# Optimization experiments

Measured on AMD Instinct MI355X. Metric: run time of the kernel, lower is better.

Reference implementation:

```python
import jax, jax.numpy as jnp
import numpy as np

N = 50000      # nodes
E = 800000     # edges (before self-loops)
IN, HID, HEADS, OUT = 128, 16, 8, 64
NEG_SLOPE = 0.2
EPS = 1e-16


def gat_layer(x, edge_index, W, att_src, att_dst, bias, heads, ch, num_nodes, concat):
    # x: [N, F_in]; edge_index: [2, E'] (row0 = source j, row1 = target i)
    h = (x @ W).reshape(-1, heads, ch)                     # [N, H, C]
    a_src = jnp.sum(h * att_src, axis=-1)                  # [N, H]
    a_dst = jnp.sum(h * att_dst, axis=-1)                  # [N, H]
    src, dst = edge_index[0], edge_index[1]
    alpha = a_src[src] + a_dst[dst]                        # [E', H]
    alpha = jax.nn.leaky_relu(alpha, NEG_SLOPE)
    # segment softmax over incoming edges of each target node
    m = jax.ops.segment_max(alpha, dst, num_segments=num_nodes)
    alpha = jnp.exp(alpha - m[dst])
    denom = jax.ops.segment_sum(alpha, dst, num_segments=num_nodes)
    alpha = alpha / (denom[dst] + EPS)
    msg = h[src] * alpha[:, :, None]                       # [E', H, C]
    out = jax.ops.segment_sum(msg, dst, num_segments=num_nodes)  # [N, H, C]
    out = out.reshape(-1, heads * ch) if concat else out.mean(axis=1)
    return out + bias


def gat_model(x, edge_index, W1, att_src1, att_dst1, b1, W2, att_src2, att_dst2, b2, num_nodes):
    # PyG GATConv default add_self_loops=True
    loops = jnp.arange(num_nodes, dtype=edge_index.dtype)
    ei = jnp.concatenate([edge_index, jnp.stack([loops, loops])], axis=1)
    h = gat_layer(x, ei, W1, att_src1, att_dst1, b1, HEADS, HID, num_nodes, concat=True)
    h = jax.nn.relu(h)
    return gat_layer(h, ei, W2, att_src2, att_dst2, b2, 1, OUT, num_nodes, concat=False)


def setup_inputs() -> dict:
    key = jax.random.key(0)
    ks = jax.random.split(key, 10)
    x = jax.random.normal(ks[0], (N, IN), jnp.float32)
    edge_index = jax.random.randint(ks[1], (2, E), 0, N, dtype=jnp.int32)
    W1 = jax.random.normal(ks[2], (IN, HEADS * HID), jnp.float32) / np.sqrt(IN).astype(np.float32)
    att_src1 = jax.random.normal(ks[3], (HEADS, HID), jnp.float32) * 0.1
    att_dst1 = jax.random.normal(ks[4], (HEADS, HID), jnp.float32) * 0.1
    b1 = jnp.zeros((HEADS * HID,), jnp.float32)
    W2 = jax.random.normal(ks[5], (HEADS * HID, OUT), jnp.float32) / np.sqrt(HEADS * HID).astype(np.float32)
    att_src2 = jax.random.normal(ks[6], (1, OUT), jnp.float32) * 0.1
    att_dst2 = jax.random.normal(ks[7], (1, OUT), jnp.float32) * 0.1
    b2 = jnp.zeros((OUT,), jnp.float32)
    return {"x": x, "edge_index": edge_index, "W1": W1, "att_src1": att_src1,
            "att_dst1": att_dst1, "b1": b1, "W2": W2, "att_src2": att_src2,
            "att_dst2": att_dst2, "b2": b2, "num_nodes": N}


def reference(x, edge_index, W1, att_src1, att_dst1, b1, W2, att_src2, att_dst2, b2, num_nodes):
    return gat_model(x, edge_index, W1, att_src1, att_dst1, b1,
                     W2, att_src2, att_dst2, b2, num_nodes)
```

## Files before the change

### kernel.cpp

```cpp
#include <hip/hip_runtime.h>

#define NEG 0.2f
#define EPSV 1e-16f
#define EPB 4096
#define CAPN 64
#define CAPB (256 * 18)

typedef _Float16 h4 __attribute__((ext_vector_type(4)));
typedef _Float16 h8 __attribute__((ext_vector_type(8)));
typedef float f32x4 __attribute__((ext_vector_type(4)));

__device__ __forceinline__ float lrelu(float x) { return x > 0.f ? x : NEG * x; }

__global__ void k_binit(int* __restrict__ bcur, int nbuckets) {
  int t = threadIdx.x;
  if (t < nbuckets) bcur[t] = t * CAPB;
}
__global__ __launch_bounds__(256) void k_bin(const int* __restrict__ src,
                                             const int* __restrict__ dst,
                                             int* __restrict__ bcur,
                                             unsigned* __restrict__ binned, int E) {
  __shared__ int hist[256];
  __shared__ int base[256];
  const int b0 = blockIdx.x * EPB;
  const int b1 = min(b0 + EPB, E);
  hist[threadIdx.x] = 0;
  __syncthreads();
  for (int e = b0 + (int)threadIdx.x; e < b1; e += 256)
    atomicAdd(&hist[dst[e] >> 8], 1);
  __syncthreads();
  int h = hist[threadIdx.x];
  if (h > 0) base[threadIdx.x] = atomicAdd(&bcur[threadIdx.x], h);
  __syncthreads();
  hist[threadIdx.x] = 0;
  __syncthreads();
  for (int e = b0 + (int)threadIdx.x; e < b1; e += 256) {
    int d = dst[e];
    int bk = d >> 8;
    int pos = base[bk] + atomicAdd(&hist[bk], 1);
    binned[pos] = ((unsigned)(d & 255) << 16) | (unsigned)src[e];
  }
}
__global__ __launch_bounds__(256) void k_unbin(const unsigned* __restrict__ binned,
                                               const int* __restrict__ bcur,
                                               unsigned short* __restrict__ csr_src,
                                               int* __restrict__ deg, int N) {
  __shared__ int cnt[256];
  const int n0 = blockIdx.x << 8;
  const int start = blockIdx.x * CAPB;
  const int end = bcur[blockIdx.x];
  cnt[threadIdx.x] = 0;
  __syncthreads();
  for (int t = start + (int)threadIdx.x; t < end; t += 256) {
    unsigned v = binned[t];
    int dl = (int)(v >> 16);
    int pos = atomicAdd(&cnt[dl], 1);
    if (pos < CAPN) csr_src[(long)(n0 + dl) * CAPN + pos] = (unsigned short)(v & 0xFFFFu);
  }
  __syncthreads();
  int n = n0 + (int)threadIdx.x;
  if (n < N) deg[n] = min(cnt[threadIdx.x], CAPN);
}

template <int M>
__global__ void k_wt(const float* __restrict__ W, _Float16* __restrict__ Wt) {
  int t = blockIdx.x * 256 + threadIdx.x;
  if (t >= M * 128) return;
  int c = t >> 7, k = t & 127;
  Wt[t] = (_Float16)W[k * M + c];
}

template <int M, int H, int C, typename TX>
__global__ __launch_bounds__(256) void k_gemm_mfma(const TX* __restrict__ X,
                                                   const _Float16* __restrict__ Wt,
                                                   const float* __restrict__ atts,
                                                   const float* __restrict__ attd,
                                                   _Float16* __restrict__ Hout,
                                                   float* __restrict__ as_,
                                                   float* __restrict__ ad_, int N) {
  constexpr int K = 128;
  constexpr int XS = 136;
  __shared__ _Float16 xs[64 * XS];
  const int tid = threadIdx.x;
  const int wv = tid >> 6, lane = tid & 63;
  const long row0 = (long)blockIdx.x * 64;
  const int nrow = (int)min((long)64, (long)N - row0);

  if constexpr (sizeof(TX) == 4) {
    for (int idx = tid; idx < 64 * (K / 4); idx += 256) {
      int r = idx >> 5, iw = idx & 31;
      float4 v = make_float4(0.f, 0.f, 0.f, 0.f);
      if (r < nrow) v = *(const float4*)&X[(row0 + r) * K + iw * 4];
      h4 o;
      o[0] = (_Float16)v.x;
      o[1] = (_Float16)v.y;
      o[2] = (_Float16)v.z;
      o[3] = (_Float16)v.w;
      *(h4*)&xs[r * XS + iw * 4] = o;
    }
  } else {
    for (int idx = tid; idx < 64 * (K / 8); idx += 256) {
      int r = idx >> 4, iw = idx & 15;
      h8 v = {};
      if (r < nrow) v = *(const h8*)&X[(row0 + r) * K + iw * 8];
      *(h8*)&xs[r * XS + iw * 8] = v;
    }
  }
  __syncthreads();

  const int rlo = lane & 15, khi = lane >> 4;
  h8 a[4];
#pragma unroll
  for (int kb = 0; kb < 4; kb++)
    a[kb] = *(const h8*)&xs[(wv * 16 + rlo) * XS + kb * 32 + khi * 8];
  __syncthreads();

  constexpr int NT = M / 16;
  const int orow = wv * 16 + khi * 4;
#pragma unroll
  for (int n = 0; n < NT; n++) {
    f32x4 acc = {0.f, 0.f, 0.f, 0.f};
#pragma unroll
    for (int kb = 0; kb < 4; kb++) {
      h8 b = *(const h8*)&Wt[(n * 16 + rlo) * K + kb * 32 + khi * 8];
      acc = __builtin_amdgcn_mfma_f32_16x16x32_f16(a[kb], b, acc, 0, 0, 0);
    }
#pragma unroll
    for (int r = 0; r < 4; r++) {
      _Float16 hv = (_Float16)acc[r];
      xs[(orow + r) * XS + n * 16 + rlo] = hv;
      if (orow + r < nrow)
        Hout[(row0 + orow + r) * M + n * 16 + rlo] = hv;
    }
  }
  __syncthreads();
  for (int t = tid; t < 64 * H; t += 256) {
    int r = t / H, h = t - r * H;
    if (r < nrow) {
      const _Float16* hp = &xs[r * XS + h * C];
      const float* sp = &atts[h * C];
      const float* dp = &attd[h * C];
      float s = 0.f, d = 0.f;
#pragma unroll
      for (int c = 0; c < C; c++) {
        float v = (float)hp[c];
        s += v * sp[c];
        d += v * dp[c];
      }
      as_[(row0 + r) * H + h] = s;
      ad_[(row0 + r) * H + h] = d;
    }
  }
}

__global__ __launch_bounds__(256) void k_node1(const int* __restrict__ deg_,
                                               const unsigned short* __restrict__ csr_src,
                                               const _Float16* __restrict__ Hf,
                                               const float* __restrict__ as_,
                                               const float* __restrict__ ad_,
                                               const float* __restrict__ bias,
                                               _Float16* __restrict__ out, int N) {
  const int wid = threadIdx.x >> 6, lane = threadIdx.x & 63;
  const int i = blockIdx.x * 4 + wid;
  if (i >= N) return;
  const long beg = (long)i * CAPN;
  const int deg = deg_[i];
  const int sub = lane >> 4, ln = lane & 15;
  const int f0 = ln * 8, hf = ln >> 1;

  const float adh = ad_[i * 8 + hf];
  const float pself = __expf(lrelu(as_[i * 8 + hf] + adh));
  float acc[8] = {0.f, 0.f, 0.f, 0.f, 0.f, 0.f, 0.f, 0.f};
  float sp = 0.f;

  int e = sub;
  for (; e + 4 < deg; e += 8) {
    int j0 = (int)csr_src[beg + e], j1 = (int)csr_src[beg + e + 4];
    float p0 = __expf(lrelu(as_[j0 * 8 + hf] + adh));
    float p1 = __expf(lrelu(as_[j1 * 8 + hf] + adh));
    h8 v0 = *(const h8*)&Hf[(long)j0 * 128 + f0];
    h8 v1 = *(const h8*)&Hf[(long)j1 * 128 + f0];
    sp += p0 + p1;
#pragma unroll
    for (int c = 0; c < 8; c++) acc[c] += p0 * (float)v0[c] + p1 * (float)v1[c];
  }
  for (; e < deg; e += 4) {
    int j = (int)csr_src[beg + e];
    float p = __expf(lrelu(as_[j * 8 + hf] + adh));
    h8 v = *(const h8*)&Hf[(long)j * 128 + f0];
    sp += p;
#pragma unroll
    for (int c = 0; c < 8; c++) acc[c] += p * (float)v[c];
  }
  if (sub == 0) {
    h8 hv = *(const h8*)&Hf[(long)i * 128 + f0];
#pragma unroll
    for (int c = 0; c < 8; c++) acc[c] += pself * (float)hv[c];
  }
  sp += __shfl_xor(sp, 16);
  sp += __shfl_xor(sp, 32);
  const float rd = 1.f / (sp + pself + EPSV);
#pragma unroll
  for (int c = 0; c < 8; c++) {
    acc[c] += __shfl_xor(acc[c], 16);
    acc[c] += __shfl_xor(acc[c], 32);
  }
  if (sub == 0) {
    h8 o;
#pragma unroll
    for (int c = 0; c < 8; c++)
      o[c] = (_Float16)fmaxf(acc[c] * rd + bias[f0 + c], 0.f);
    *(h8*)&out[(long)i * 128 + f0] = o;
  }
}

__global__ __launch_bounds__(256) void k_node2(const int* __restrict__ deg_,
                                               const unsigned short* __restrict__ csr_src,
                                               const _Float16* __restrict__ Hf,
                                               const float* __restrict__ as_,
                                               const float* __restrict__ ad_,
                                               const float* __restrict__ bias,
                                               float* __restrict__ out, int N) {
  const int wid = threadIdx.x >> 6, lane = threadIdx.x & 63;
  const int i = blockIdx.x * 4 + wid;
  if (i >= N) return;
  const long beg = (long)i * CAPN;
  const int deg = deg_[i];
  const int sub = lane >> 3, ln = lane & 7;
  const int f0 = ln * 8;

  const float adi = ad_[i];
  const float pself = __expf(lrelu(as_[i] + adi));
  float acc[8] = {0.f, 0.f, 0.f, 0.f, 0.f, 0.f, 0.f, 0.f};
  float sp = 0.f;

  int e = sub;
  for (; e + 8 < deg; e += 16) {
    int j0 = (int)csr_src[beg + e], j1 = (int)csr_src[beg + e + 8];
    float p0 = __expf(lrelu(as_[j0] + adi));
    float p1 = __expf(lrelu(as_[j1] + adi));
    h8 v0 = *(const h8*)&Hf[(long)j0 * 64 + f0];
    h8 v1 = *(const h8*)&Hf[(long)j1 * 64 + f0];
    sp += p0 + p1;
#pragma unroll
    for (int c = 0; c < 8; c++) acc[c] += p0 * (float)v0[c] + p1 * (float)v1[c];
  }
  for (; e < deg; e += 8) {
    int j = (int)csr_src[beg + e];
    float p = __expf(lrelu(as_[j] + adi));
    h8 v = *(const h8*)&Hf[(long)j * 64 + f0];
    sp += p;
#pragma unroll
    for (int c = 0; c < 8; c++) acc[c] += p * (float)v[c];
  }
  if (sub == 0) {
    h8 hv = *(const h8*)&Hf[(long)i * 64 + f0];
#pragma unroll
    for (int c = 0; c < 8; c++) acc[c] += pself * (float)hv[c];
  }
  sp += __shfl_xor(sp, 8);
  sp += __shfl_xor(sp, 16);
  sp += __shfl_xor(sp, 32);
  const float rd = 1.f / (sp + pself + EPSV);
#pragma unroll
  for (int c = 0; c < 8; c++) {
    acc[c] += __shfl_xor(acc[c], 8);
    acc[c] += __shfl_xor(acc[c], 16);
    acc[c] += __shfl_xor(acc[c], 32);
  }
  if (sub == 0) {
    float4 b0 = *(const float4*)&bias[f0];
    float4 b1 = *(const float4*)&bias[f0 + 4];
    float4 o0, o1;
    o0.x = acc[0] * rd + b0.x;
    o0.y = acc[1] * rd + b0.y;
    o0.z = acc[2] * rd + b0.z;
    o0.w = acc[3] * rd + b0.w;
    o1.x = acc[4] * rd + b1.x;
    o1.y = acc[5] * rd + b1.y;
    o1.z = acc[6] * rd + b1.z;
    o1.w = acc[7] * rd + b1.w;
    *(float4*)&out[(long)i * 64 + f0] = o0;
    *(float4*)&out[(long)i * 64 + f0 + 4] = o1;
  }
}

extern "C" void kernel_launch(void* const* d_in, const int* in_sizes, int n_in,
                              void* d_out, int out_size, void* d_ws, size_t ws_size,
                              hipStream_t stream) {
  const float* x = (const float*)d_in[0];
  const int* ei = (const int*)d_in[1];
  const float* W1 = (const float*)d_in[2];
  const float* s1 = (const float*)d_in[3];
  const float* dd1 = (const float*)d_in[4];
  const float* b1 = (const float*)d_in[5];
  const float* W2 = (const float*)d_in[6];
  const float* s2 = (const float*)d_in[7];
  const float* dd2 = (const float*)d_in[8];
  const float* b2 = (const float*)d_in[9];
  const int N = in_sizes[0] / 128;
  const int E = in_sizes[1] / 2;
  const int* src = ei;
  const int* dst = ei + E;
  const int nbuckets = (N + 255) >> 8;

  char* wsp = (char*)d_ws;
  _Float16* Wt1 = (_Float16*)wsp;
  _Float16* Wt2 = Wt1 + 128 * 128;
  _Float16* Hh = Wt2 + 64 * 128;
  float* as1 = (float*)((char*)Hh + (size_t)N * 128 * sizeof(_Float16));
  float* ad1 = as1 + (size_t)N * 8;
  _Float16* X2h = (_Float16*)(ad1 + (size_t)N * 8);
  int* deg = (int*)(X2h + (size_t)N * 128);
  unsigned short* csr_src = (unsigned short*)(deg + N);
  int* bcur = (int*)(csr_src + (size_t)N * CAPN);
  unsigned* binned = (unsigned*)(bcur + 256);
  float* out = (float*)d_out;

  dim3 B(256);
  auto nb = [](long n) { return dim3((unsigned)((n + 255) / 256)); };

  k_wt<128><<<dim3(64), B, 0, stream>>>(W1, Wt1);
  k_wt<64><<<dim3(32), B, 0, stream>>>(W2, Wt2);

  k_binit<<<dim3(1), B, 0, stream>>>(bcur, nbuckets);
  k_bin<<<dim3((E + EPB - 1) / EPB), B, 0, stream>>>(src, dst, bcur, binned, E);
  k_unbin<<<dim3(nbuckets), B, 0, stream>>>(binned, bcur, csr_src, deg, N);

  k_gemm_mfma<128, 8, 16, float><<<dim3((N + 63) / 64), B, 0, stream>>>(
      x, Wt1, s1, dd1, Hh, as1, ad1, N);
  k_node1<<<dim3((N + 3) / 4), B, 0, stream>>>(deg, csr_src, Hh, as1, ad1, b1, X2h, N);

  k_gemm_mfma<64, 1, 64, _Float16><<<dim3((N + 63) / 64), B, 0, stream>>>(
      X2h, Wt2, s2, dd2, Hh, as1, ad1, N);
  k_node2<<<dim3((N + 3) / 4), B, 0, stream>>>(deg, csr_src, Hh, as1, ad1, b2, out, N);
}
```

Before: 143.7 us.

## Fuse setup kernels, co-schedule binning with GEMM1, fuse node1 aggregation into GEMM2

Merges the two weight transposes and bucket init into one setup kernel. Runs edge binning and the first GEMM as disjoint block ranges of one launch, since neither depends on the other. Fuses layer-1 aggregation with the layer-2 GEMM so each block aggregates 64 nodes into shared memory and multiplies them by W2 directly, which removes the X2h round trip and two launches. The cost is that the fused node kernel now has only N/64 blocks, each wave handling 16 nodes in sequence, so parallelism and latency hiding for the gather-heavy aggregation drop.

Measured after the change: 140.5 us. -2.2%, faster.

```diff
diff --git a/kernel.cpp b/kernel.cpp
--- a/kernel.cpp
+++ b/kernel.cpp
@@ -12,35 +12,119 @@
 
 __device__ __forceinline__ float lrelu(float x) { return x > 0.f ? x : NEG * x; }
 
-__global__ void k_binit(int* __restrict__ bcur, int nbuckets) {
-  int t = threadIdx.x;
-  if (t < nbuckets) bcur[t] = t * CAPB;
-}
-__global__ __launch_bounds__(256) void k_bin(const int* __restrict__ src,
-                                             const int* __restrict__ dst,
-                                             int* __restrict__ bcur,
-                                             unsigned* __restrict__ binned, int E) {
-  __shared__ int hist[256];
-  __shared__ int base[256];
-  const int b0 = blockIdx.x * EPB;
-  const int b1 = min(b0 + EPB, E);
-  hist[threadIdx.x] = 0;
-  __syncthreads();
-  for (int e = b0 + (int)threadIdx.x; e < b1; e += 256)
-    atomicAdd(&hist[dst[e] >> 8], 1);
-  __syncthreads();
-  int h = hist[threadIdx.x];
-  if (h > 0) base[threadIdx.x] = atomicAdd(&bcur[threadIdx.x], h);
-  __syncthreads();
-  hist[threadIdx.x] = 0;
-  __syncthreads();
-  for (int e = b0 + (int)threadIdx.x; e < b1; e += 256) {
-    int d = dst[e];
-    int bk = d >> 8;
-    int pos = base[bk] + atomicAdd(&hist[bk], 1);
-    binned[pos] = ((unsigned)(d & 255) << 16) | (unsigned)src[e];
-  }
-}
+__global__ void k_setup(const float* __restrict__ W1, _Float16* __restrict__ Wt1,
+                        const float* __restrict__ W2, _Float16* __restrict__ Wt2,
+                        int* __restrict__ bcur, int nbuckets) {
+  const int bid = blockIdx.x, tid = threadIdx.x;
+  if (bid < 64) {
+    int t = bid * 256 + tid;
+    int c = t >> 7, k = t & 127;
+    Wt1[t] = (_Float16)W1[k * 128 + c];
+  } else if (bid < 96) {
+    int t = (bid - 64) * 256 + tid;
+    if (t < 64 * 128) {
+      int c = t >> 7, k = t & 127;
+      Wt2[t] = (_Float16)W2[k * 64 + c];
+    }
+  } else {
+    if (tid < nbuckets) bcur[tid] = tid * CAPB;
+  }
+}
+
+__global__ __launch_bounds__(256) void k_bin_gemm1(
+    const int* __restrict__ src, const int* __restrict__ dst, int* __restrict__ bcur,
+    unsigned* __restrict__ binned, int E, int nBinB, const float* __restrict__ X,
+    const _Float16* __restrict__ Wt, const float* __restrict__ atts,
+    const float* __restrict__ attd, _Float16* __restrict__ Hout,
+    float* __restrict__ as_, float* __restrict__ ad_, int N) {
+  constexpr int K = 128, XS = 136;
+  __shared__ _Float16 xs[64 * XS];
+  const int tid = threadIdx.x;
+
+  if ((int)blockIdx.x < nBinB) {
+    int* hist = (int*)xs;
+    int* base = hist + 256;
+    const int b0 = blockIdx.x * EPB;
+    const int b1 = min(b0 + EPB, E);
+    hist[tid] = 0;
+    __syncthreads();
+    for (int e = b0 + tid; e < b1; e += 256) atomicAdd(&hist[dst[e] >> 8], 1);
+    __syncthreads();
+    int h = hist[tid];
+    if (h > 0) base[tid] = atomicAdd(&bcur[tid], h);
+    __syncthreads();
+    hist[tid] = 0;
+    __syncthreads();
+    for (int e = b0 + tid; e < b1; e += 256) {
+      int d = dst[e];
+      int bk = d >> 8;
+      int pos = base[bk] + atomicAdd(&hist[bk], 1);
+      binned[pos] = ((unsigned)(d & 255) << 16) | (unsigned)src[e];
+    }
+    return;
+  }
+
+  const int bid = blockIdx.x - nBinB;
+  const int wv = tid >> 6, lane = tid & 63;
+  const long row0 = (long)bid * 64;
+  const int nrow = (int)min((long)64, (long)N - row0);
+
+  for (int idx = tid; idx < 64 * (K / 4); idx += 256) {
+    int r = idx >> 5, iw = idx & 31;
+    float4 v = make_float4(0.f, 0.f, 0.f, 0.f);
+    if (r < nrow) v = *(const float4*)&X[(row0 + r) * K + iw * 4];
+    h4 o;
+    o[0] = (_Float16)v.x;
+    o[1] = (_Float16)v.y;
+    o[2] = (_Float16)v.z;
+    o[3] = (_Float16)v.w;
+    *(h4*)&xs[r * XS + iw * 4] = o;
+  }
+  __syncthreads();
+
+  const int rlo = lane & 15, khi = lane >> 4;
+  h8 a[4];
+#pragma unroll
+  for (int kb = 0; kb < 4; kb++)
+    a[kb] = *(const h8*)&xs[(wv * 16 + rlo) * XS + kb * 32 + khi * 8];
+  __syncthreads();
+
+  const int orow = wv * 16 + khi * 4;
+#pragma unroll
+  for (int n = 0; n < 8; n++) {
+    f32x4 acc = {0.f, 0.f, 0.f, 0.f};
+#pragma unroll
+    for (int kb = 0; kb < 4; kb++) {
+      h8 b = *(const h8*)&Wt[(n * 16 + rlo) * K + kb * 32 + khi * 8];
+      acc = __builtin_amdgcn_mfma_f32_16x16x32_f16(a[kb], b, acc, 0, 0, 0);
+    }
+#pragma unroll
+    for (int r = 0; r < 4; r++) {
+      _Float16 hv = (_Float16)acc[r];
+      xs[(orow + r) * XS + n * 16 + rlo] = hv;
+      if (orow + r < nrow) Hout[(row0 + orow + r) * 128 + n * 16 + rlo] = hv;
+    }
+  }
+  __syncthreads();
+  for (int t = tid; t < 64 * 8; t += 256) {
+    int r = t >> 3, h = t & 7;
+    if (r < nrow) {
+      const _Float16* hp = &xs[r * XS + h * 16];
+      const float* sp = &atts[h * 16];
+      const float* dp = &attd[h * 16];
+      float s = 0.f, d = 0.f;
+#pragma unroll
+      for (int c = 0; c < 16; c++) {
+        float v = (float)hp[c];
+        s += v * sp[c];
+        d += v * dp[c];
+      }
+      as_[(row0 + r) * 8 + h] = s;
+      ad_[(row0 + r) * 8 + h] = d;
+    }
+  }
+}
+
 __global__ __launch_bounds__(256) void k_unbin(const unsigned* __restrict__ binned,
                                                const int* __restrict__ bcur,
                                                unsigned short* __restrict__ csr_src,
@@ -62,48 +146,74 @@
   if (n < N) deg[n] = min(cnt[threadIdx.x], CAPN);
 }
 
-template <int M>
-__global__ void k_wt(const float* __restrict__ W, _Float16* __restrict__ Wt) {
-  int t = blockIdx.x * 256 + threadIdx.x;
-  if (t >= M * 128) return;
-  int c = t >> 7, k = t & 127;
-  Wt[t] = (_Float16)W[k * M + c];
-}
-
-template <int M, int H, int C, typename TX>
-__global__ __launch_bounds__(256) void k_gemm_mfma(const TX* __restrict__ X,
-                                                   const _Float16* __restrict__ Wt,
-                                                   const float* __restrict__ atts,
-                                                   const float* __restrict__ attd,
-                                                   _Float16* __restrict__ Hout,
-                                                   float* __restrict__ as_,
-                                                   float* __restrict__ ad_, int N) {
-  constexpr int K = 128;
-  constexpr int XS = 136;
+__global__ __launch_bounds__(256) void k_n1g2(
+    const int* __restrict__ deg_, const unsigned short* __restrict__ csr_src,
+    const _Float16* __restrict__ Hf, const float* __restrict__ as1,
+    const float* __restrict__ ad1, const float* __restrict__ b1,
+    const _Float16* __restrict__ Wt2, const float* __restrict__ s2,
+    const float* __restrict__ dd2, _Float16* __restrict__ H2,
+    float* __restrict__ as2, float* __restrict__ ad2, int N) {
+  constexpr int K = 128, XS = 136;
   __shared__ _Float16 xs[64 * XS];
   const int tid = threadIdx.x;
   const int wv = tid >> 6, lane = tid & 63;
   const long row0 = (long)blockIdx.x * 64;
   const int nrow = (int)min((long)64, (long)N - row0);
-
-  if constexpr (sizeof(TX) == 4) {
-    for (int idx = tid; idx < 64 * (K / 4); idx += 256) {
-      int r = idx >> 5, iw = idx & 31;
-      float4 v = make_float4(0.f, 0.f, 0.f, 0.f);
-      if (r < nrow) v = *(const float4*)&X[(row0 + r) * K + iw * 4];
-      h4 o;
-      o[0] = (_Float16)v.x;
-      o[1] = (_Float16)v.y;
-      o[2] = (_Float16)v.z;
-      o[3] = (_Float16)v.w;
-      *(h4*)&xs[r * XS + iw * 4] = o;
-    }
-  } else {
-    for (int idx = tid; idx < 64 * (K / 8); idx += 256) {
-      int r = idx >> 4, iw = idx & 15;
-      h8 v = {};
-      if (r < nrow) v = *(const h8*)&X[(row0 + r) * K + iw * 8];
-      *(h8*)&xs[r * XS + iw * 8] = v;
+  const int sub = lane >> 4, ln = lane & 15;
+  const int f0 = ln * 8, hf = ln >> 1;
+
+  for (int t = 0; t < 16; t++) {
+    const int r = wv * 16 + t;
+    const long i = row0 + r;
+    if (i < N) {
+      const int deg = deg_[i];
+      const long beg = i * CAPN;
+      const float adh = ad1[i * 8 + hf];
+      const float pself = __expf(lrelu(as1[i * 8 + hf] + adh));
+      float acc[8] = {0.f, 0.f, 0.f, 0.f, 0.f, 0.f, 0.f, 0.f};
+      float sp = 0.f;
+      int e = sub;
+      for (; e + 4 < deg; e += 8) {
+        int j0 = (int)csr_src[beg + e], j1 = (int)csr_src[beg + e + 4];
+        float p0 = __expf(lrelu(as1[j0 * 8 + hf] + adh));
+        float p1 = __expf(lrelu(as1[j1 * 8 + hf] + adh));
+        h8 v0 = *(const h8*)&Hf[(long)j0 * 128 + f0];
+        h8 v1 = *(const h8*)&Hf[(long)j1 * 128 + f0];
+        sp += p0 + p1;
+#pragma unroll
+        for (int c = 0; c < 8; c++) acc[c] += p0 * (float)v0[c] + p1 * (float)v1[c];
+      }
+      for (; e < deg; e += 4) {
+        int j = (int)csr_src[beg + e];
+        float p = __expf(lrelu(as1[j * 8 + hf] + adh));
+        h8 v = *(const h8*)&Hf[(long)j * 128 + f0];
+        sp += p;
+#pragma unroll
+        for (int c = 0; c < 8; c++) acc[c] += p * (float)v[c];
+      }
+      if (sub == 0) {
+        h8 hv = *(const h8*)&Hf[i * 128 + f0];
+#pragma unroll
+        for (int c = 0; c < 8; c++) acc[c] += pself * (float)hv[c];
+      }
+      sp += __shfl_xor(sp, 16);
+      sp += __shfl_xor(sp, 32);
+      const float rd = 1.f / (sp + pself + EPSV);
+#pragma unroll
+      for (int c = 0; c < 8; c++) {
+        acc[c] += __shfl_xor(acc[c], 16);
+        acc[c] += __shfl_xor(acc[c], 32);
+      }
+      if (sub == 0) {
+        h8 o;
+#pragma unroll
+        for (int c = 0; c < 8; c++)
+          o[c] = (_Float16)fmaxf(acc[c] * rd + b1[f0 + c], 0.f);
+        *(h8*)&xs[r * XS + f0] = o;
+      }
+    } else if (sub == 0) {
+      h8 z = {};
+      *(h8*)&xs[r * XS + f0] = z;
     }
   }
   __syncthreads();
@@ -115,102 +225,36 @@
     a[kb] = *(const h8*)&xs[(wv * 16 + rlo) * XS + kb * 32 + khi * 8];
   __syncthreads();
 
-  constexpr int NT = M / 16;
   const int orow = wv * 16 + khi * 4;
 #pragma unroll
-  for (int n = 0; n < NT; n++) {
+  for (int n = 0; n < 4; n++) {
     f32x4 acc = {0.f, 0.f, 0.f, 0.f};
 #pragma unroll
     for (int kb = 0; kb < 4; kb++) {
-      h8 b = *(const h8*)&Wt[(n * 16 + rlo) * K + kb * 32 + khi * 8];
+      h8 b = *(const h8*)&Wt2[(n * 16 + rlo) * K + kb * 32 + khi * 8];
       acc = __builtin_amdgcn_mfma_f32_16x16x32_f16(a[kb], b, acc, 0, 0, 0);
     }
 #pragma unroll
     for (int r = 0; r < 4; r++) {
       _Float16 hv = (_Float16)acc[r];
       xs[(orow + r) * XS + n * 16 + rlo] = hv;
-      if (orow + r < nrow)
-        Hout[(row0 + orow + r) * M + n * 16 + rlo] = hv;
-    }
-  }
-  __syncthreads();
-  for (int t = tid; t < 64 * H; t += 256) {
-    int r = t / H, h = t - r * H;
-    if (r < nrow) {
-      const _Float16* hp = &xs[r * XS + h * C];
-      const float* sp = &atts[h * C];
-      const float* dp = &attd[h * C];
+      if (orow + r < nrow) H2[(row0 + orow + r) * 64 + n * 16 + rlo] = hv;
+    }
+  }
+  __syncthreads();
+  for (int t = tid; t < 64; t += 256) {
+    if (t < nrow) {
+      const _Float16* hp = &xs[t * XS];
       float s = 0.f, d = 0.f;
 #pragma unroll
-      for (int c = 0; c < C; c++) {
+      for (int c = 0; c < 64; c++) {
         float v = (float)hp[c];
-        s += v * sp[c];
-        d += v * dp[c];
-      }
-      as_[(row0 + r) * H + h] = s;
-      ad_[(row0 + r) * H + h] = d;
-    }
-  }
-}
-
-__global__ __launch_bounds__(256) void k_node1(const int* __restrict__ deg_,
-                                               const unsigned short* __restrict__ csr_src,
-                                               const _Float16* __restrict__ Hf,
-                                               const float* __restrict__ as_,
-                                               const float* __restrict__ ad_,
-                                               const float* __restrict__ bias,
-                                               _Float16* __restrict__ out, int N) {
-  const int wid = threadIdx.x >> 6, lane = threadIdx.x & 63;
-  const int i = blockIdx.x * 4 + wid;
-  if (i >= N) return;
-  const long beg = (long)i * CAPN;
-  const int deg = deg_[i];
-  const int sub = lane >> 4, ln = lane & 15;
-  const int f0 = ln * 8, hf = ln >> 1;
-
-  const float adh = ad_[i * 8 + hf];
-  const float pself = __expf(lrelu(as_[i * 8 + hf] + adh));
-  float acc[8] = {0.f, 0.f, 0.f, 0.f, 0.f, 0.f, 0.f, 0.f};
-  float sp = 0.f;
-
-  int e = sub;
-  for (; e + 4 < deg; e += 8) {
-    int j0 = (int)csr_src[beg + e], j1 = (int)csr_src[beg + e + 4];
-    float p0 = __expf(lrelu(as_[j0 * 8 + hf] + adh));
-    float p1 = __expf(lrelu(as_[j1 * 8 + hf] + adh));
-    h8 v0 = *(const h8*)&Hf[(long)j0 * 128 + f0];
-    h8 v1 = *(const h8*)&Hf[(long)j1 * 128 + f0];
-    sp += p0 + p1;
-#pragma unroll
-    for (int c = 0; c < 8; c++) acc[c] += p0 * (float)v0[c] + p1 * (float)v1[c];
-  }
-  for (; e < deg; e += 4) {
-    int j = (int)csr_src[beg + e];
-    float p = __expf(lrelu(as_[j * 8 + hf] + adh));
-    h8 v = *(const h8*)&Hf[(long)j * 128 + f0];
-    sp += p;
-#pragma unroll
-    for (int c = 0; c < 8; c++) acc[c] += p * (float)v[c];
-  }
-  if (sub == 0) {
-    h8 hv = *(const h8*)&Hf[(long)i * 128 + f0];
-#pragma unroll
-    for (int c = 0; c < 8; c++) acc[c] += pself * (float)hv[c];
-  }
-  sp += __shfl_xor(sp, 16);
-  sp += __shfl_xor(sp, 32);
-  const float rd = 1.f / (sp + pself + EPSV);
-#pragma unroll
-  for (int c = 0; c < 8; c++) {
-    acc[c] += __shfl_xor(acc[c], 16);
-    acc[c] += __shfl_xor(acc[c], 32);
-  }
-  if (sub == 0) {
-    h8 o;
-#pragma unroll
-    for (int c = 0; c < 8; c++)
-      o[c] = (_Float16)fmaxf(acc[c] * rd + bias[f0 + c], 0.f);
-    *(h8*)&out[(long)i * 128 + f0] = o;
+        s += v * s2[c];
+        d += v * dd2[c];
+      }
+      as2[row0 + t] = s;
+      ad2[row0 + t] = d;
+    }
   }
 }
 
@@ -303,6 +347,8 @@
   const int* src = ei;
   const int* dst = ei + E;
   const int nbuckets = (N + 255) >> 8;
+  const int nBinB = (E + EPB - 1) / EPB;
+  const int nGemmB = (N + 63) / 64;
 
   char* wsp = (char*)d_ws;
   _Float16* Wt1 = (_Float16*)wsp;
@@ -310,28 +356,26 @@
   _Float16* Hh = Wt2 + 64 * 128;
   float* as1 = (float*)((char*)Hh + (size_t)N * 128 * sizeof(_Float16));
   float* ad1 = as1 + (size_t)N * 8;
-  _Float16* X2h = (_Float16*)(ad1 + (size_t)N * 8);
-  int* deg = (int*)(X2h + (size_t)N * 128);
+  _Float16* H2 = (_Float16*)(ad1 + (size_t)N * 8);
+  float* as2 = (float*)(H2 + (size_t)N * 64);
+  float* ad2 = as2 + N;
+  int* deg = (int*)(ad2 + N);
   unsigned short* csr_src = (unsigned short*)(deg + N);
   int* bcur = (int*)(csr_src + (size_t)N * CAPN);
   unsigned* binned = (unsigned*)(bcur + 256);
   float* out = (float*)d_out;
 
   dim3 B(256);
-  auto nb = [](long n) { return dim3((unsigned)((n + 255) / 256)); };
-
-  k_wt<128><<<dim3(64), B, 0, stream>>>(W1, Wt1);
-  k_wt<64><<<dim3(32), B, 0, stream>>>(W2, Wt2);
-
-  k_binit<<<dim3(1), B, 0, stream>>>(bcur, nbuckets);
-  k_bin<<<dim3((E + EPB - 1) / EPB), B, 0, stream>>>(src, dst, bcur, binned, E);
+
+  k_setup<<<dim3(97), B, 0, stream>>>(W1, Wt1, W2, Wt2, bcur, nbuckets);
+
+  k_bin_gemm1<<<dim3(nBinB + nGemmB), B, 0, stream>>>(
+      src, dst, bcur, binned, E, nBinB, x, Wt1, s1, dd1, Hh, as1, ad1, N);
+
   k_unbin<<<dim3(nbuckets), B, 0, stream>>>(binned, bcur, csr_src, deg, N);
 
-  k_gemm_mfma<128, 8, 16, float><<<dim3((N + 63) / 64), B, 0, stream>>>(
-      x, Wt1, s1, dd1, Hh, as1, ad1, N);
-  k_node1<<<dim3((N + 3) / 4), B, 0, stream>>>(deg, csr_src, Hh, as1, ad1, b1, X2h, N);
-
-  k_gemm_mfma<64, 1, 64, _Float16><<<dim3((N + 63) / 64), B, 0, stream>>>(
-      X2h, Wt2, s2, dd2, Hh, as1, ad1, N);
-  k_node2<<<dim3((N + 3) / 4), B, 0, stream>>>(deg, csr_src, Hh, as1, ad1, b2, out, N);
-}
+  k_n1g2<<<dim3(nGemmB), B, 0, stream>>>(deg, csr_src, Hh, as1, ad1, b1, Wt2, s2, dd2,
+                                         H2, as2, ad2, N);
+
+  k_node2<<<dim3((N + 3) / 4), B, 0, stream>>>(deg, csr_src, H2, as2, ad2, b2, out, N);
+}
```
